# Optimization experiments

Measured on AMD Instinct MI355X. Metric: run time of the kernel, lower is better.

The kernel has to match this reference:

```python
import jax, jax.numpy as jnp
import numpy as np
import math

D_MODEL = 1024
N_HEADS = 16
D_K = D_MODEL // N_HEADS
MAX_LEN = 200
B, S = 64, 200


def _temporal_bias():
    # bias[i, j] = -0.1 * |i - j| / max_len, same for every head
    idx = jnp.arange(MAX_LEN, dtype=jnp.float32)
    dist = jnp.abs(idx[:, None] - idx[None, :])  # [L, L]
    tb = (-0.1 * dist / MAX_LEN)[None, None, :, :]  # [1, 1, L, L]
    return jnp.broadcast_to(tb, (1, N_HEADS, MAX_LEN, MAX_LEN))


def setup_inputs() -> dict:
    key = jax.random.key(0)
    ks = jax.random.split(key, 9)
    lim = 1.0 / math.sqrt(D_MODEL)
    def lin_w(k):
        return jax.random.uniform(k, (D_MODEL, D_MODEL), jnp.float32, -lim, lim)
    def lin_b(k):
        return jax.random.uniform(k, (D_MODEL,), jnp.float32, -lim, lim)
    return {
        "x": jax.random.normal(ks[0], (B, S, D_MODEL), jnp.float32),
        "mask": jnp.ones((B, 1, S, S), jnp.int32),
        "wq": lin_w(ks[1]), "bq": lin_b(ks[2]),
        "wk": lin_w(ks[3]), "bk": lin_b(ks[4]),
        "wv": lin_w(ks[5]), "bv": lin_b(ks[6]),
        "wo": lin_w(ks[7]), "bo": lin_b(ks[8]),
        "temporal_bias": _temporal_bias(),
    }


def reference(x, mask, wq, bq, wk, bk, wv, bv, wo, bo, temporal_bias):
    b, s, d = x.shape
    h, dk = N_HEADS, D_K
    scale = math.sqrt(dk)
    # torch Linear: y = x @ W.T + b; heads: [b, s, h, dk] -> [b, h, s, dk]
    q = (jnp.einsum('bsd,ed->bse', x, wq) + bq).reshape(b, s, h, dk).transpose(0, 2, 1, 3)
    k = (jnp.einsum('bsd,ed->bse', x, wk) + bk).reshape(b, s, h, dk).transpose(0, 2, 1, 3)
    v = (jnp.einsum('bsd,ed->bse', x, wv) + bv).reshape(b, s, h, dk).transpose(0, 2, 1, 3)
    scores = jnp.einsum('bhqd,bhkd->bhqk', q, k) / scale  # [b, h, s, s]
    scores = scores + temporal_bias[:, :, :s, :s]
    scores = jnp.where(mask == 0, jnp.float32(-1e9), scores)
    attn = jax.nn.softmax(scores, axis=-1)  # dropout is identity in eval mode
    ctx = jnp.einsum('bhqk,bhkd->bhqd', attn, v)
    ctx = ctx.transpose(0, 2, 1, 3).reshape(b, s, d)
    out = jnp.einsum('bsd,ed->bse', ctx, wo) + bo
    return out, attn
```

## Files before the change

### kernel.cpp

```cpp
#include <hip/hip_runtime.h>
#include <stdint.h>

typedef unsigned short u16;
typedef __bf16 bf16x8 __attribute__((ext_vector_type(8)));
typedef float f32x4 __attribute__((ext_vector_type(4)));

#define MFMA16(a, b, c) __builtin_amdgcn_mfma_f32_16x16x32_bf16((a), (b), (c), 0, 0, 0)

#define BB 64
#define SS 200
#define DM 1024
#define NH 16
#define DKK 64
#define MM (BB * SS)
#define OUT0_ELEMS (MM * DM)

__device__ static inline u16 f2bf(float f) {
    __bf16 h = (__bf16)f;
    return __builtin_bit_cast(u16, h);
}

__device__ static inline bf16x8 load8(const u16* p) {
    uint4 u = *(const uint4*)p;
    union { uint4 u; bf16x8 b; } cv; cv.u = u; return cv.b;
}

__device__ static inline bf16x8 bzero8() {
    union { uint4 u; bf16x8 b; } cv; cv.u = make_uint4(0u, 0u, 0u, 0u); return cv.b;
}

__device__ static inline void gload_lds16(const void* g, void* l) {
    __builtin_amdgcn_global_load_lds(
        (const __attribute__((address_space(1))) void*)g,
        (__attribute__((address_space(3))) void*)l, 16, 0, 0);
}

__global__ __launch_bounds__(256) void convert_k(
    const float* __restrict__ x,
    const float* __restrict__ wq, const float* __restrict__ wk,
    const float* __restrict__ wv, const float* __restrict__ wo,
    u16* __restrict__ xb,
    u16* __restrict__ wqb, u16* __restrict__ wkb,
    u16* __restrict__ wvb, u16* __restrict__ wob)
{
    size_t i4 = (size_t)blockIdx.x * 256 + threadIdx.x;
    size_t e = i4 * 4;
    const float* src; u16* dst; size_t off;
    if (e < (size_t)OUT0_ELEMS) { src = x; dst = xb; off = e; }
    else {
        size_t we = e - OUT0_ELEMS;
        size_t w = we >> 20;
        off = we & 1048575u;
        src = (w == 0) ? wq : (w == 1) ? wk : (w == 2) ? wv : wo;
        dst = (w == 0) ? wqb : (w == 1) ? wkb : (w == 2) ? wvb : wob;
    }
    float4 v = *(const float4*)(src + off);
    union { u16 s[4]; uint2 u; } o;
    o.s[0] = f2bf(v.x); o.s[1] = f2bf(v.y); o.s[2] = f2bf(v.z); o.s[3] = f2bf(v.w);
    *(uint2*)(dst + off) = o.u;
}

template <int MODE>
__global__ __launch_bounds__(256) void gemm_k(
    const u16* __restrict__ A,
    const u16* __restrict__ W0, const u16* __restrict__ W1, const u16* __restrict__ W2,
    const float* __restrict__ b0, const float* __restrict__ b1, const float* __restrict__ b2,
    u16* __restrict__ qo, u16* __restrict__ ko, u16* __restrict__ vto,
    float* __restrict__ outf)
{
    __shared__ __align__(16) u16 As[128 * 32];
    __shared__ __align__(16) u16 Bs[128 * 32];

    const int tid  = threadIdx.x;
    const int wave = tid >> 6;
    const int lane = tid & 63;
    const int quad = lane >> 4;
    const int l15  = lane & 15;
    const int n0   = blockIdx.x * 128;
    const int m0   = blockIdx.y * 128;
    const int z    = (MODE == 0) ? blockIdx.z : 0;

    const u16* W = (MODE == 1) ? W0 : (z == 0 ? W0 : (z == 1 ? W1 : W2));
    const float* bias = (MODE == 1) ? b0 : (z == 0 ? b0 : (z == 1 ? b1 : b2));

    const int srow = wave * 16 + (lane >> 2);
    const int sk8  = (lane & 3) * 8;
    const int wuni = __builtin_amdgcn_readfirstlane(wave);

    f32x4 acc[4][4];
#pragma unroll
    for (int i = 0; i < 4; i++)
#pragma unroll
        for (int j = 0; j < 4; j++) acc[i][j] = (f32x4){0.f, 0.f, 0.f, 0.f};

    const int wr = (wave >> 1) * 64;
    const int wc = (wave & 1) * 64;

    const u16* Ag = A + (size_t)m0 * 1024;
    const u16* Wg = W + (size_t)n0 * 1024;

    for (int kc = 0; kc < 1024; kc += 32) {
        __syncthreads();
#pragma unroll
        for (int r = 0; r < 2; r++) {
            int row = r * 64 + srow;
            gload_lds16(Ag + (size_t)row * 1024 + kc + sk8, &As[(r * 64 + wuni * 16) * 32]);
        }
#pragma unroll
        for (int r = 0; r < 2; r++) {
            int row = r * 64 + srow;
            gload_lds16(Wg + (size_t)row * 1024 + kc + sk8, &Bs[(r * 64 + wuni * 16) * 32]);
        }
        __syncthreads();

        bf16x8 af[4], bf[4];
#pragma unroll
        for (int mt = 0; mt < 4; mt++) af[mt] = load8(&As[(wr + mt * 16 + l15) * 32 + quad * 8]);
#pragma unroll
        for (int nt = 0; nt < 4; nt++) bf[nt] = load8(&Bs[(wc + nt * 16 + l15) * 32 + quad * 8]);
#pragma unroll
        for (int mt = 0; mt < 4; mt++)
#pragma unroll
            for (int nt = 0; nt < 4; nt++)
                acc[mt][nt] = MFMA16(af[mt], bf[nt], acc[mt][nt]);
    }

#pragma unroll
    for (int nt = 0; nt < 4; nt++) {
        int n = n0 + wc + nt * 16 + l15;
        float bv = bias[n];
#pragma unroll
        for (int mt = 0; mt < 4; mt++) {
#pragma unroll
            for (int r = 0; r < 4; r++) {
                int m = m0 + wr + mt * 16 + quad * 4 + r;
                float val = acc[mt][nt][r] + bv;
                if (MODE == 0) {
                    int b = m / 200, s = m - b * 200;
                    int h = n >> 6, d = n & 63;
                    size_t bh = (size_t)(b * 16 + h);
                    if (z == 0)      qo[(bh * 200 + s) * 64 + d] = f2bf(val);
                    else if (z == 1) ko[(bh * 200 + s) * 64 + d] = f2bf(val);
                    else             vto[(bh * 64 + d) * 200 + s] = f2bf(val);
                } else {
                    outf[(size_t)m * 1024 + n] = val;
                }
            }
        }
    }
}

__global__ __launch_bounds__(256) void attn_k(
    const u16* __restrict__ qg, const u16* __restrict__ kg, const u16* __restrict__ vt,
    const float* __restrict__ tb, const int* __restrict__ mask,
    float* __restrict__ attn_out, u16* __restrict__ ctxb)
{
    __shared__ __align__(16) u16 Ap[4 * 16 * 224];

    const int tid  = threadIdx.x;
    const int wave = tid >> 6;
    const int lane = tid & 63;
    const int quad = lane >> 4;
    const int l15  = lane & 15;
    const int bh   = blockIdx.y;
    const int b    = bh >> 4;
    const int h    = bh & 15;
    const int i0   = blockIdx.x * 64 + wave * 16;

    const u16* qp = qg + (size_t)bh * 200 * 64;
    const u16* kp = kg + (size_t)bh * 200 * 64;

    int qi = i0 + l15;
    bf16x8 aq0, aq1;
    if (qi < 200) {
        aq0 = load8(qp + qi * 64 + quad * 8);
        aq1 = load8(qp + qi * 64 + 32 + quad * 8);
    } else { aq0 = bzero8(); aq1 = bzero8(); }

    f32x4 sc[13];
#pragma unroll
    for (int t = 0; t < 13; t++) {
        int kj = t * 16 + l15;
        bf16x8 bk0, bk1;
        if (kj < 200) {
            bk0 = load8(kp + kj * 64 + quad * 8);
            bk1 = load8(kp + kj * 64 + 32 + quad * 8);
        } else { bk0 = bzero8(); bk1 = bzero8(); }
        f32x4 zz = (f32x4){0.f, 0.f, 0.f, 0.f};
        zz = MFMA16(aq0, bk0, zz);
        zz = MFMA16(aq1, bk1, zz);
        sc[t] = zz;
    }

    const int ibase = i0 + quad * 4;
    const float* tbp = tb + (size_t)h * 40000 + (size_t)ibase * 200 + l15;
    const int*   mkp = mask + (size_t)b * 40000 + (size_t)ibase * 200 + l15;

    float mx[4] = {-3e38f, -3e38f, -3e38f, -3e38f};
#pragma unroll
    for (int t = 0; t < 13; t++) {
#pragma unroll
        for (int r = 0; r < 4; r++) {
            int i = ibase + r, j = t * 16 + l15;
            float s;
            if (i < 200 && j < 200) {
                s = sc[t][r] * 0.125f + tbp[r * 200 + t * 16];
                if (mkp[r * 200 + t * 16] == 0) s = -1e9f;
            } else s = -3e38f;
            sc[t][r] = s;
            mx[r] = fmaxf(mx[r], s);
        }
    }
#pragma unroll
    for (int r = 0; r < 4; r++)
        for (int m = 1; m < 16; m <<= 1) mx[r] = fmaxf(mx[r], __shfl_xor(mx[r], m, 64));

    float sum[4] = {0.f, 0.f, 0.f, 0.f};
#pragma unroll
    for (int t = 0; t < 13; t++) {
#pragma unroll
        for (int r = 0; r < 4; r++) {
            int i = ibase + r, j = t * 16 + l15;
            float e = (i < 200 && j < 200) ? __expf(sc[t][r] - mx[r]) : 0.f;
            sc[t][r] = e;
            sum[r] += e;
        }
    }
#pragma unroll
    for (int r = 0; r < 4; r++)
        for (int m = 1; m < 16; m <<= 1) sum[r] += __shfl_xor(sum[r], m, 64);

    float inv[4];
#pragma unroll
    for (int r = 0; r < 4; r++) inv[r] = (sum[r] > 0.f) ? 1.f / sum[r] : 0.f;

    u16* lp = &Ap[wave * 16 * 224];
    float* aop = attn_out + ((size_t)bh * 200 + ibase) * 200 + l15;
#pragma unroll
    for (int t = 0; t < 13; t++) {
#pragma unroll
        for (int r = 0; r < 4; r++) {
            int i = ibase + r, j = t * 16 + l15;
            float a = sc[t][r] * inv[r];
            lp[(quad * 4 + r) * 224 + j] = f2bf(a);
            if (i < 200 && j < 200) aop[r * 200 + t * 16] = a;
        }
    }
#pragma unroll
    for (int r = 0; r < 4; r++) lp[(quad * 4 + r) * 224 + 208 + l15] = 0;
    __syncthreads();

    f32x4 ctx[4];
#pragma unroll
    for (int nt = 0; nt < 4; nt++) ctx[nt] = (f32x4){0.f, 0.f, 0.f, 0.f};
    const u16* vtb = vt + (size_t)bh * 64 * 200;
#pragma unroll
    for (int kc = 0; kc < 224; kc += 32) {
        bf16x8 af = load8(lp + l15 * 224 + kc + quad * 8);
        int j0 = kc + quad * 8;
#pragma unroll
        for (int nt = 0; nt < 4; nt++) {
            bf16x8 bv = (j0 < 200) ? load8(vtb + (nt * 16 + l15) * 200 + j0) : bzero8();
            ctx[nt] = MFMA16(af, bv, ctx[nt]);
        }
    }

#pragma unroll
    for (int nt = 0; nt < 4; nt++) {
#pragma unroll
        for (int r = 0; r < 4; r++) {
            int i = ibase + r;
            if (i < 200)
                ctxb[((size_t)b * 200 + i) * 1024 + h * 64 + nt * 16 + l15] = f2bf(ctx[nt][r]);
        }
    }
}

extern "C" void kernel_launch(void* const* d_in, const int* in_sizes, int n_in,
                              void* d_out, int out_size, void* d_ws, size_t ws_size,
                              hipStream_t stream) {
    const float* x    = (const float*)d_in[0];
    const int*   mask = (const int*)d_in[1];
    const float* wq   = (const float*)d_in[2];
    const float* bq   = (const float*)d_in[3];
    const float* wk   = (const float*)d_in[4];
    const float* bk   = (const float*)d_in[5];
    const float* wv   = (const float*)d_in[6];
    const float* bv   = (const float*)d_in[7];
    const float* wo   = (const float*)d_in[8];
    const float* bo   = (const float*)d_in[9];
    const float* tb   = (const float*)d_in[10];

    float* out  = (float*)d_out;
    float* attn = out + OUT0_ELEMS;

    char* ws = (char*)d_ws;
    u16* xb   = (u16*)(ws);
    u16* wqb  = (u16*)(ws + 26214400);
    u16* wkb  = (u16*)(ws + 28311552);
    u16* wvb  = (u16*)(ws + 30408704);
    u16* wob  = (u16*)(ws + 32505856);
    u16* qb   = (u16*)(ws + 34603008);
    u16* kb   = (u16*)(ws + 60817408);
    u16* vtb  = (u16*)(ws + 87031808);
    u16* ctxb = (u16*)(ws + 113246208);

    convert_k<<<dim3(16896), dim3(256), 0, stream>>>(x, wq, wk, wv, wo, xb, wqb, wkb, wvb, wob);

    gemm_k<0><<<dim3(8, 100, 3), dim3(256), 0, stream>>>(
        xb, wqb, wkb, wvb, bq, bk, bv, qb, kb, vtb, nullptr);

    attn_k<<<dim3(4, 1024), dim3(256), 0, stream>>>(qb, kb, vtb, tb, mask, attn, ctxb);

    gemm_k<1><<<dim3(8, 100, 1), dim3(256), 0, stream>>>(
        ctxb, wob, nullptr, nullptr, bo, nullptr, nullptr, nullptr, nullptr, nullptr, out);
}
```

Baseline: 665.3 us.

## Pack mask to bits, vectorize attention softmax stores via LDS, pack V^T writes

Adds a pre-pass that compresses the int32 mask into 64-bit bitmasks so the attention kernel reads far less mask data. The attention kernel now stages scores through LDS so each lane owns a row segment and can use float4 loads of the bias and float4 stores of the attention matrix, with coalesced 16-byte writes of the context. The V-transpose epilogue in the QKV GEMM packs four bf16 values per store. Costs an extra kernel launch plus more LDS per block, and waves with no valid rows exit early, which skips the block-wide barrier.

```diff
diff --git a/kernel.cpp b/kernel.cpp
--- a/kernel.cpp
+++ b/kernel.cpp
@@ -2,6 +2,7 @@
 #include <stdint.h>
 
 typedef unsigned short u16;
+typedef unsigned long long u64;
 typedef __bf16 bf16x8 __attribute__((ext_vector_type(8)));
 typedef float f32x4 __attribute__((ext_vector_type(4)));
 
@@ -11,7 +12,6 @@
 #define SS 200
 #define DM 1024
 #define NH 16
-#define DKK 64
 #define MM (BB * SS)
 #define OUT0_ELEMS (MM * DM)
 
@@ -60,6 +60,30 @@
     *(uint2*)(dst + off) = o.u;
 }
 
+__global__ __launch_bounds__(256) void maskbits_k(
+    const int* __restrict__ mask, u64* __restrict__ bits)
+{
+    __shared__ unsigned char nb[4][64];
+    const int wave = threadIdx.x >> 6, lane = threadIdx.x & 63;
+    const int row = blockIdx.x * 4 + wave;
+    if (row >= MM / DM * 0 + BB * SS) {  }
+    const int* mp = mask + (size_t)row * 200;
+    unsigned nib;
+    if (lane < 50) {
+        int4 v = *(const int4*)(mp + lane * 4);
+        nib = (v.x ? 1u : 0u) | (v.y ? 2u : 0u) | (v.z ? 4u : 0u) | (v.w ? 8u : 0u);
+    } else nib = 0xFu;
+    nb[wave][lane] = (unsigned char)nib;
+    __builtin_amdgcn_s_waitcnt(0);
+    if (lane < 4) {
+        const unsigned char* p = &nb[wave][lane * 16];
+        u64 m = 0;
+#pragma unroll
+        for (int i = 0; i < 16; i++) m |= (u64)(p[i] & 0xFu) << (4 * i);
+        bits[(size_t)row * 4 + lane] = m;
+    }
+}
+
 template <int MODE>
 __global__ __launch_bounds__(256) void gemm_k(
     const u16* __restrict__ A,
@@ -131,19 +155,28 @@
         float bv = bias[n];
 #pragma unroll
         for (int mt = 0; mt < 4; mt++) {
-#pragma unroll
-            for (int r = 0; r < 4; r++) {
-                int m = m0 + wr + mt * 16 + quad * 4 + r;
-                float val = acc[mt][nt][r] + bv;
-                if (MODE == 0) {
-                    int b = m / 200, s = m - b * 200;
-                    int h = n >> 6, d = n & 63;
-                    size_t bh = (size_t)(b * 16 + h);
-                    if (z == 0)      qo[(bh * 200 + s) * 64 + d] = f2bf(val);
-                    else if (z == 1) ko[(bh * 200 + s) * 64 + d] = f2bf(val);
-                    else             vto[(bh * 64 + d) * 200 + s] = f2bf(val);
-                } else {
-                    outf[(size_t)m * 1024 + n] = val;
+            if (MODE == 0 && z == 2) {
+                int mbase = m0 + wr + mt * 16 + quad * 4;
+                int b = mbase / 200, s = mbase - b * 200;
+                int hh = n >> 6, d = n & 63;
+                union { u16 q[4]; uint2 u; } pk;
+#pragma unroll
+                for (int r = 0; r < 4; r++) pk.q[r] = f2bf(acc[mt][nt][r] + bv);
+                *(uint2*)&vto[((size_t)(b * 16 + hh) * 64 + d) * 200 + s] = pk.u;
+            } else {
+#pragma unroll
+                for (int r = 0; r < 4; r++) {
+                    int m = m0 + wr + mt * 16 + quad * 4 + r;
+                    float val = acc[mt][nt][r] + bv;
+                    if (MODE == 0) {
+                        int b = m / 200, s = m - b * 200;
+                        int hh = n >> 6, d = n & 63;
+                        size_t bhid = (size_t)(b * 16 + hh);
+                        if (z == 0) qo[(bhid * 200 + s) * 64 + d] = f2bf(val);
+                        else        ko[(bhid * 200 + s) * 64 + d] = f2bf(val);
+                    } else {
+                        outf[(size_t)m * 1024 + n] = val;
+                    }
                 }
             }
         }
@@ -151,11 +184,12 @@
 }
 
 __global__ __launch_bounds__(256) void attn_k(
-    const u16* __restrict__ qg, const u16* __restrict__ kg, const u16* __restrict__ vt,
-    const float* __restrict__ tb, const int* __restrict__ mask,
+    const u16* __restrict__ qg, const u16* __restrict__ kg, const u16* __restrict__ vtg,
+    const float* __restrict__ tb, const u64* __restrict__ mbits,
     float* __restrict__ attn_out, u16* __restrict__ ctxb)
 {
-    __shared__ __align__(16) u16 Ap[4 * 16 * 224];
+    __shared__ __align__(16) float Sf[4][16 * 212];
+    __shared__ __align__(16) u16  Pb[4][16 * 208];
 
     const int tid  = threadIdx.x;
     const int wave = tid >> 6;
@@ -166,9 +200,12 @@
     const int b    = bh >> 4;
     const int h    = bh & 15;
     const int i0   = blockIdx.x * 64 + wave * 16;
+    if (i0 >= 200) return;
 
     const u16* qp = qg + (size_t)bh * 200 * 64;
     const u16* kp = kg + (size_t)bh * 200 * 64;
+    float* sf = Sf[wave];
+    u16*   pb = Pb[wave];
 
     int qi = i0 + l15;
     bf16x8 aq0, aq1;
@@ -177,7 +214,6 @@
         aq1 = load8(qp + qi * 64 + 32 + quad * 8);
     } else { aq0 = bzero8(); aq1 = bzero8(); }
 
-    f32x4 sc[13];
 #pragma unroll
     for (int t = 0; t < 13; t++) {
         int kj = t * 16 + l15;
@@ -186,93 +222,100 @@
             bk0 = load8(kp + kj * 64 + quad * 8);
             bk1 = load8(kp + kj * 64 + 32 + quad * 8);
         } else { bk0 = bzero8(); bk1 = bzero8(); }
-        f32x4 zz = (f32x4){0.f, 0.f, 0.f, 0.f};
-        zz = MFMA16(aq0, bk0, zz);
-        zz = MFMA16(aq1, bk1, zz);
-        sc[t] = zz;
-    }
-
-    const int ibase = i0 + quad * 4;
-    const float* tbp = tb + (size_t)h * 40000 + (size_t)ibase * 200 + l15;
-    const int*   mkp = mask + (size_t)b * 40000 + (size_t)ibase * 200 + l15;
-
-    float mx[4] = {-3e38f, -3e38f, -3e38f, -3e38f};
-#pragma unroll
-    for (int t = 0; t < 13; t++) {
-#pragma unroll
-        for (int r = 0; r < 4; r++) {
-            int i = ibase + r, j = t * 16 + l15;
-            float s;
-            if (i < 200 && j < 200) {
-                s = sc[t][r] * 0.125f + tbp[r * 200 + t * 16];
-                if (mkp[r * 200 + t * 16] == 0) s = -1e9f;
-            } else s = -3e38f;
-            sc[t][r] = s;
-            mx[r] = fmaxf(mx[r], s);
+        f32x4 z = (f32x4){0.f, 0.f, 0.f, 0.f};
+        z = MFMA16(aq0, bk0, z);
+        z = MFMA16(aq1, bk1, z);
+#pragma unroll
+        for (int r = 0; r < 4; r++) sf[(quad * 4 + r) * 212 + t * 16 + l15] = z[r];
+    }
+
+    const int row = lane >> 2, sub = lane & 3;
+    const int iabs = i0 + row;
+    const bool rowok = iabs < 200;
+    const int irow = rowok ? iabs : 0;
+    const u64* mb = mbits + ((size_t)b * 200 + irow) * 4;
+    ulonglong2 mA = *(const ulonglong2*)mb;
+    ulonglong2 mB = *(const ulonglong2*)(mb + 2);
+    const float* tbrow = tb + (size_t)h * 40000 + (size_t)irow * 200;
+
+    f32x4 sv[13];
+    float mx = -3.0e38f;
+#pragma unroll
+    for (int c = 0; c < 13; c++) {
+        int col = c * 16 + sub * 4;
+        f32x4 s = *(const f32x4*)&sf[row * 212 + col];
+        if (rowok && col < 200) {
+            float4 tv = *(const float4*)(tbrow + col);
+            u64 ch = (col < 64) ? mA.x : (col < 128) ? mA.y : (col < 192) ? mB.x : mB.y;
+            int sh = col & 63;
+            s[0] = s[0] * 0.125f + tv.x; if (!((ch >> (sh + 0)) & 1)) s[0] = -1e9f;
+            s[1] = s[1] * 0.125f + tv.y; if (!((ch >> (sh + 1)) & 1)) s[1] = -1e9f;
+            s[2] = s[2] * 0.125f + tv.z; if (!((ch >> (sh + 2)) & 1)) s[2] = -1e9f;
+            s[3] = s[3] * 0.125f + tv.w; if (!((ch >> (sh + 3)) & 1)) s[3] = -1e9f;
+        } else { s[0] = s[1] = s[2] = s[3] = -3.0e38f; }
+        sv[c] = s;
+        mx = fmaxf(mx, fmaxf(fmaxf(s[0], s[1]), fmaxf(s[2], s[3])));
+    }
+    mx = fmaxf(mx, __shfl_xor(mx, 1, 64));
+    mx = fmaxf(mx, __shfl_xor(mx, 2, 64));
+
+    float sum = 0.f;
+#pragma unroll
+    for (int c = 0; c < 13; c++) {
+        f32x4 s = sv[c];
+        s[0] = __expf(s[0] - mx); s[1] = __expf(s[1] - mx);
+        s[2] = __expf(s[2] - mx); s[3] = __expf(s[3] - mx);
+        sv[c] = s;
+        sum += (s[0] + s[1]) + (s[2] + s[3]);
+    }
+    sum += __shfl_xor(sum, 1, 64);
+    sum += __shfl_xor(sum, 2, 64);
+    float inv = (sum > 0.f) ? 1.f / sum : 0.f;
+
+    float* aop = attn_out + ((size_t)bh * 200 + irow) * 200;
+#pragma unroll
+    for (int c = 0; c < 13; c++) {
+        int col = c * 16 + sub * 4;
+        f32x4 a = sv[c];
+        a[0] *= inv; a[1] *= inv; a[2] *= inv; a[3] *= inv;
+        union { u16 q[4]; uint2 u; } pk;
+        if (col < 200) {
+            pk.q[0] = f2bf(a[0]); pk.q[1] = f2bf(a[1]);
+            pk.q[2] = f2bf(a[2]); pk.q[3] = f2bf(a[3]);
+        } else pk.u = make_uint2(0u, 0u);
+        *(uint2*)&pb[row * 208 + col] = pk.u;
+        if (rowok && col < 200)
+            *(float4*)(aop + col) = make_float4(a[0], a[1], a[2], a[3]);
+    }
+
+    f32x4 ctx[4];
+#pragma unroll
+    for (int nt = 0; nt < 4; nt++) ctx[nt] = (f32x4){0.f, 0.f, 0.f, 0.f};
+    const u16* vb = vtg + (size_t)bh * 64 * 200;
+#pragma unroll
+    for (int kc = 0; kc < 224; kc += 32) {
+        int j0 = kc + quad * 8;
+        bf16x8 af = (j0 < 208) ? load8(pb + l15 * 208 + j0) : bzero8();
+#pragma unroll
+        for (int nt = 0; nt < 4; nt++) {
+            bf16x8 bvf = (j0 < 200) ? load8(vb + (nt * 16 + l15) * 200 + j0) : bzero8();
+            ctx[nt] = MFMA16(af, bvf, ctx[nt]);
         }
     }
-#pragma unroll
-    for (int r = 0; r < 4; r++)
-        for (int m = 1; m < 16; m <<= 1) mx[r] = fmaxf(mx[r], __shfl_xor(mx[r], m, 64));
-
-    float sum[4] = {0.f, 0.f, 0.f, 0.f};
-#pragma unroll
-    for (int t = 0; t < 13; t++) {
-#pragma unroll
-        for (int r = 0; r < 4; r++) {
-            int i = ibase + r, j = t * 16 + l15;
-            float e = (i < 200 && j < 200) ? __expf(sc[t][r] - mx[r]) : 0.f;
-            sc[t][r] = e;
-            sum[r] += e;
-        }
-    }
-#pragma unroll
-    for (int r = 0; r < 4; r++)
-        for (int m = 1; m < 16; m <<= 1) sum[r] += __shfl_xor(sum[r], m, 64);
-
-    float inv[4];
-#pragma unroll
-    for (int r = 0; r < 4; r++) inv[r] = (sum[r] > 0.f) ? 1.f / sum[r] : 0.f;
-
-    u16* lp = &Ap[wave * 16 * 224];
-    float* aop = attn_out + ((size_t)bh * 200 + ibase) * 200 + l15;
-#pragma unroll
-    for (int t = 0; t < 13; t++) {
-#pragma unroll
-        for (int r = 0; r < 4; r++) {
-            int i = ibase + r, j = t * 16 + l15;
-            float a = sc[t][r] * inv[r];
-            lp[(quad * 4 + r) * 224 + j] = f2bf(a);
-            if (i < 200 && j < 200) aop[r * 200 + t * 16] = a;
-        }
-    }
-#pragma unroll
-    for (int r = 0; r < 4; r++) lp[(quad * 4 + r) * 224 + 208 + l15] = 0;
-    __syncthreads();
-
-    f32x4 ctx[4];
-#pragma unroll
-    for (int nt = 0; nt < 4; nt++) ctx[nt] = (f32x4){0.f, 0.f, 0.f, 0.f};
-    const u16* vtb = vt + (size_t)bh * 64 * 200;
-#pragma unroll
-    for (int kc = 0; kc < 224; kc += 32) {
-        bf16x8 af = load8(lp + l15 * 224 + kc + quad * 8);
-        int j0 = kc + quad * 8;
-#pragma unroll
-        for (int nt = 0; nt < 4; nt++) {
-            bf16x8 bv = (j0 < 200) ? load8(vtb + (nt * 16 + l15) * 200 + j0) : bzero8();
-            ctx[nt] = MFMA16(af, bv, ctx[nt]);
-        }
-    }
-
-#pragma unroll
-    for (int nt = 0; nt < 4; nt++) {
-#pragma unroll
-        for (int r = 0; r < 4; r++) {
-            int i = ibase + r;
-            if (i < 200)
-                ctxb[((size_t)b * 200 + i) * 1024 + h * 64 + nt * 16 + l15] = f2bf(ctx[nt][r]);
-        }
+
+#pragma unroll
+    for (int nt = 0; nt < 4; nt++)
+#pragma unroll
+        for (int r = 0; r < 4; r++)
+            pb[(quad * 4 + r) * 208 + nt * 16 + l15] = f2bf(ctx[nt][r]);
+
+#pragma unroll
+    for (int k = 0; k < 2; k++) {
+        int rr = k * 8 + (lane >> 3), ss = lane & 7;
+        int ia = i0 + rr;
+        uint4 val = *(const uint4*)&pb[rr * 208 + ss * 8];
+        if (ia < 200)
+            *(uint4*)&ctxb[((size_t)b * 200 + ia) * 1024 + h * 64 + ss * 8] = val;
     }
 }
 
@@ -295,22 +338,25 @@
     float* attn = out + OUT0_ELEMS;
 
     char* ws = (char*)d_ws;
-    u16* xb   = (u16*)(ws);
-    u16* wqb  = (u16*)(ws + 26214400);
-    u16* wkb  = (u16*)(ws + 28311552);
-    u16* wvb  = (u16*)(ws + 30408704);
-    u16* wob  = (u16*)(ws + 32505856);
-    u16* qb   = (u16*)(ws + 34603008);
-    u16* kb   = (u16*)(ws + 60817408);
-    u16* vtb  = (u16*)(ws + 87031808);
-    u16* ctxb = (u16*)(ws + 113246208);
+    u16* xb    = (u16*)(ws);
+    u16* wqb   = (u16*)(ws + 26214400);
+    u16* wkb   = (u16*)(ws + 28311552);
+    u16* wvb   = (u16*)(ws + 30408704);
+    u16* wob   = (u16*)(ws + 32505856);
+    u16* qb    = (u16*)(ws + 34603008);
+    u16* kb    = (u16*)(ws + 60817408);
+    u16* vtb   = (u16*)(ws + 87031808);
+    u16* ctxb  = (u16*)(ws + 113246208);
+    u64* mbits = (u64*)(ws + 139460608);
 
     convert_k<<<dim3(16896), dim3(256), 0, stream>>>(x, wq, wk, wv, wo, xb, wqb, wkb, wvb, wob);
+
+    maskbits_k<<<dim3(3200), dim3(256), 0, stream>>>(mask, mbits);
 
     gemm_k<0><<<dim3(8, 100, 3), dim3(256), 0, stream>>>(
         xb, wqb, wkb, wvb, bq, bk, bv, qb, kb, vtb, nullptr);
 
-    attn_k<<<dim3(4, 1024), dim3(256), 0, stream>>>(qb, kb, vtb, tb, mask, attn, ctxb);
+    attn_k<<<dim3(4, 1024), dim3(256), 0, stream>>>(qb, kb, vtb, tb, mbits, attn, ctxb);
 
     gemm_k<1><<<dim3(8, 100, 1), dim3(256), 0, stream>>>(
         ctxb, wob, nullptr, nullptr, bo, nullptr, nullptr, nullptr, nullptr, nullptr, out);
```

Measured after the change: 587.6 us. -11.7%, faster.
